# Performance work log

Hardware: AMD Instinct MI355X
Metric: run time of the kernel (lower is better)

Reference implementation:

```python
import jax, jax.numpy as jnp
import numpy as np

ALPHA, BETA = 0.5, 0.25
DELTA_AGG, DELTA_DIS = 0.5, 3.0
OHEM_RATIO = 3
MAX_INST = 8  # instance ids in [0, MAX_INST); 0 = background
NEG_INF = -1e10


def _safe_norm(sq):
    # sqrt with zero-safe gradient; returns 0 where sq == 0
    return jnp.sqrt(jnp.where(sq > 0, sq, 1.0)) * (sq > 0)


def _agg_dis_single(sim, gt_text, gt_kernel):
    # sim: [4, N] float, gt_text/gt_kernel: [N] int32 instance ids
    lab = jnp.arange(1, MAX_INST)                                  # [K]
    kmask = (gt_kernel[None, :] == lab[:, None]).astype(sim.dtype)  # [K, N]
    tmask = gt_text[None, :] == lab[:, None]                        # [K, N] bool
    kcount = kmask.sum(1)
    tcount = tmask.sum(1).astype(sim.dtype)
    valid = (kcount > 0) & (tcount > 0)                             # [K]
    # per-instance kernel centroid G_kernel: masked segment mean of sim vectors
    G = (kmask @ sim.T) / jnp.maximum(kcount, 1.0)[:, None]         # [K, 4]
    # loss_agg: distance of each text pixel's sim vector to its kernel centroid
    diff = sim.T[None, :, :] - G[:, None, :]                        # [K, N, 4]
    d = _safe_norm(jnp.sum(diff * diff, -1))                        # [K, N]
    D = jnp.square(jnp.maximum(d - DELTA_AGG, 0.0))
    per_inst = jnp.sum(jnp.log1p(D) * tmask, 1) / jnp.maximum(tcount, 1.0)
    n_valid = jnp.sum(valid)
    loss_agg = jnp.sum(jnp.where(valid, per_inst, 0.0)) / jnp.maximum(n_valid, 1).astype(sim.dtype)
    # loss_dis: pairwise discrimination between valid kernel centroids
    gd = G[:, None, :] - G[None, :, :]                              # [K, K, 4]
    gnorm = _safe_norm(jnp.sum(gd * gd, -1))
    Dij = jnp.square(jnp.maximum(DELTA_DIS - gnorm, 0.0))
    K = MAX_INST - 1
    idx = jnp.arange(K)
    pair = valid[:, None] & valid[None, :] & (idx[:, None] < idx[None, :])
    s = jnp.sum(jnp.where(pair, jnp.log1p(Dij), 0.0))
    denom = (n_valid * (n_valid - 1)).astype(sim.dtype)  # matches torch: n*(n-1), not #pairs
    loss_dis = jnp.where(n_valid > 1, s / jnp.maximum(denom, 1.0), 0.0)
    return loss_agg, loss_dis


def _ohem_single(score, gt, tm):
    # score/tm: [N] float, gt: [N] int — all flattened
    pos = gt > 0.5
    pos_num = jnp.sum(pos) - jnp.sum(pos & (tm <= 0.5))
    neg = ~pos
    neg_total = jnp.sum(neg)
    neg_num = jnp.minimum(pos_num * OHEM_RATIO, neg_total)
    neg_scores = jnp.where(neg, score, NEG_INF)
    sorted_desc = -jnp.sort(-neg_scores)
    threshold = sorted_desc[jnp.maximum(neg_num - 1, 0)]
    sel = (((score >= threshold) | pos) & (tm > 0.5)).astype(tm.dtype)
    fallback = (pos_num == 0) | (neg_num == 0)
    return jnp.where(fallback, tm, sel)


def _dice(inp, tgt, mask):
    # inp: [B, N] logits, tgt: [B, N] (binarized at 0.5), mask: [B, N]
    p = jax.nn.sigmoid(inp) * mask
    t = (tgt > 0.5).astype(p.dtype) * mask
    a = jnp.sum(p * t, 1)
    b = jnp.sum(p * p, 1) + 1e-3
    c = jnp.sum(t * t, 1) + 1e-3
    return 1.0 - 2.0 * a / (b + c)


def _pan_loss(outputs, labels, training_masks):
    B = outputs.shape[0]
    texts = outputs[:, 0].reshape(B, -1)
    kernels = outputs[:, 1].reshape(B, -1)
    sim = outputs[:, 2:].reshape(B, 4, -1)
    gt_texts = labels[:, 0].reshape(B, -1)
    gt_kernels = labels[:, 1].reshape(B, -1)
    tm = training_masks.reshape(B, -1)

    loss_aggs, loss_diss = jax.vmap(_agg_dis_single)(sim, gt_texts, gt_kernels)

    # OHEM mask is computed on detached scores in the original (numpy round-trip)
    sel_text = jax.vmap(_ohem_single)(jax.lax.stop_gradient(texts), gt_texts, tm)
    loss_texts = _dice(texts, gt_texts, sel_text)

    sel_kernel = jax.lax.stop_gradient(
        ((jax.nn.sigmoid(texts) > 0.5) & (tm > 0.5)).astype(texts.dtype))
    loss_kernels = _dice(kernels, gt_kernels, sel_kernel)

    loss_text = loss_texts.mean()
    loss_kernel = loss_kernels.mean()
    loss_agg = loss_aggs.mean()
    loss_dis = loss_diss.mean()
    loss_all = loss_text + ALPHA * loss_kernel + BETA * (loss_agg + loss_dis)
    return loss_all, loss_text, loss_kernel, loss_agg, loss_dis


def setup_inputs() -> dict:
    key = jax.random.key(0)
    k1, k2, k3 = jax.random.split(key, 3)
    B, H, W = 8, 640, 640
    outputs = jax.random.normal(k1, (B, 6, H, W), dtype=jnp.float32)
    labels = jax.random.randint(k2, (B, 2, H, W), 0, MAX_INST).astype(jnp.int32)
    training_masks = jax.random.uniform(k3, (B, H, W), dtype=jnp.float32)
    return {"outputs": outputs, "labels": labels, "training_masks": training_masks}


def reference(outputs, labels, training_masks):
    return _pan_loss(outputs, labels, training_masks)
```

## Files before the change

kernel.cpp:

```cpp
#include <hip/hip_runtime.h>

#define NPIX 409600
#define NB 8

constexpr int OFF_H0   = 0;
constexpr int OFF_H1   = 2048;
constexpr int OFF_H2   = 4096;
constexpr int OFF_KC   = 5120;
constexpr int OFF_TC   = 5128;
constexpr int OFF_KS   = 5136;
constexpr int OFF_AGG  = 5168;
constexpr int OFF_CPOS = 5176;
constexpr int OFF_CPOSM= 5177;
constexpr int OFF_KN   = 5178;
constexpr int OFF_KNF  = 5179;
constexpr int OFF_FALL = 5180;
constexpr int OFF_NV   = 5181;
constexpr int OFF_VM   = 5182;
constexpr int OFF_LDIS = 5183;
constexpr int OFF_BTN  = 5184;
constexpr int OFF_PFX0 = 5185;
constexpr int OFF_K1   = 5186;
constexpr int OFF_PFX22= 5187;
constexpr int OFF_K2   = 5188;
constexpr int OFF_DICE = 5190;
constexpr int PER_BATCH= 5248;
constexpr int KEYS_BASE= NB * PER_BATCH;
constexpr int HDR_WORDS= NB * PER_BATCH;

__device__ __forceinline__ unsigned mapf(float s) {
  unsigned b = __float_as_uint(s);
  return (b & 0x80000000u) ? ~b : (b | 0x80000000u);
}
__device__ __forceinline__ float unmapf(unsigned u) {
  return __uint_as_float((u & 0x80000000u) ? (u & 0x7FFFFFFFu) : ~u);
}
__device__ __forceinline__ float sigf(float x) {
  return __fdividef(1.f, 1.f + __expf(-x));
}
__device__ __forceinline__ float wredf(float v) {
#pragma unroll
  for (int m = 32; m >= 1; m >>= 1) v += __shfl_xor(v, m, 64);
  return v;
}
__device__ __forceinline__ unsigned wredu(unsigned v) {
#pragma unroll
  for (int m = 32; m >= 1; m >>= 1) v += (unsigned)__shfl_xor((int)v, m, 64);
  return v;
}

__global__ __launch_bounds__(256) void kZ(unsigned* __restrict__ ws) {
  int i = blockIdx.x * 256 + threadIdx.x;
  if (i < HDR_WORDS) ws[i] = 0u;
}

__global__ __launch_bounds__(256) void kXS(const float* __restrict__ out_,
                                           const int* __restrict__ lab_,
                                           const float* __restrict__ tm_,
                                           unsigned* __restrict__ ws) {
  const int b = blockIdx.y;
  unsigned* wsb = ws + (size_t)b * PER_BATCH;
  float* wsbf = (float*)wsb;
  __shared__ __align__(16) unsigned shm[2384];
  const int tid = threadIdx.x, lane = tid & 63, w = tid >> 6;

  if (blockIdx.x < 200) {
    const int bx = blockIdx.x;
    unsigned* sh_h   = shm;
    unsigned* shScan = shm + 2048;
    unsigned* shTC   = shm + 2304;
    float*    shRed  = (float*)(shm + 2332);
    unsigned* shC    = shm + 2368;
    unsigned* shBase = shm + 2376;
    for (int i = tid; i < 2048; i += 256) sh_h[i] = 0u;
    __syncthreads();

    const float4* tx = (const float4*)(out_ + (size_t)b * 6 * NPIX);
    const float4* kr = (const float4*)(out_ + (size_t)b * 6 * NPIX + (size_t)NPIX);
    const int4* gt = (const int4*)(lab_ + (size_t)b * 2 * NPIX);
    const int4* gk = (const int4*)(lab_ + (size_t)b * 2 * NPIX + NPIX);
    const float4* tmv = (const float4*)(tm_ + (size_t)b * NPIX);

    unsigned cpos = 0, cposm = 0, vmask = 0, fmask = 0;
    unsigned tcq[7];
#pragma unroll
    for (int k = 0; k < 7; ++k) tcq[k] = 0u;
    unsigned kreg[8];
    float at = 0.f, btp = 0.f, ct = 0.f, atf = 0.f, btf = 0.f, ctf = 0.f;
    float ak = 0.f, bk = 0.f, ck = 0.f;

#pragma unroll
    for (int it = 0; it < 2; ++it) {
      const int i = it * 51200 + bx * 256 + tid;
      float4 t4 = tx[i]; float4 q4 = kr[i]; int4 g4 = gt[i]; int4 k4 = gk[i]; float4 m4 = tmv[i];
#pragma unroll
      for (int j = 0; j < 4; ++j) {
        float tv = ((const float*)&t4)[j];
        float kv = ((const float*)&q4)[j];
        int gtv = ((const int*)&g4)[j];
        int gkv = ((const int*)&k4)[j];
        float mv = ((const float*)&m4)[j];
        bool pos = gtv > 0;
        bool mh = mv > 0.5f;
        cpos += pos;
        cposm += (pos && !mh);
        unsigned key = mapf(tv);
        kreg[it * 4 + j] = key;
        float sig = sigf(tv);
        if (!pos) {
          vmask |= 1u << (it * 4 + j);
          if (mh) fmask |= 1u << (it * 4 + j);
          atomicAdd(&sh_h[key >> 21], 1u);
        } else if (mh) {
          at += sig; btp += sig * sig; ct += 1.f;
        }
#pragma unroll
        for (int k = 0; k < 7; ++k)
          tcq[k] += (gtv == k + 1);
        float sm = sig * mv;
        btf += sm * sm;
        if (pos) { atf += sm * mv; ctf += mv * mv; }
        if ((tv > 0.f) && mh) {
          float sk = sigf(kv);
          bk += sk * sk;
          if (gkv > 0) { ak += sk; ck += 1.f; }
        }
      }
    }

    unsigned r = wredu(cpos), r2 = wredu(cposm);
    if (lane == 0) { shC[w * 2] = r; shC[w * 2 + 1] = r2; }
#pragma unroll
    for (int k = 0; k < 7; ++k) {
      unsigned rt = wredu(tcq[k]);
      if (lane == 0) shTC[w * 7 + k] = rt;
    }
    float v9[9] = {at, btp, ct, atf, btf, ctf, ak, bk, ck};
#pragma unroll
    for (int q = 0; q < 9; ++q) {
      float f = wredf(v9[q]);
      if (lane == 0) shRed[w * 9 + q] = f;
    }

    unsigned cnt = (unsigned)__popc(vmask), cntF = (unsigned)__popc(fmask);
    shScan[tid] = cnt | (cntF << 16);
    __syncthreads();
#pragma unroll
    for (int off = 1; off < 256; off <<= 1) {
      unsigned vv = (tid >= off) ? shScan[tid - off] : 0u;
      __syncthreads();
      shScan[tid] += vv;
      __syncthreads();
    }
    if (tid == 0) {
      unsigned tot = shScan[255];
      shBase[0] = atomicAdd(&wsb[OFF_KN], tot & 0xFFFFu);
      shBase[1] = atomicAdd(&wsb[OFF_KNF], tot >> 16);
    }
    for (int i = tid; i < 2048; i += 256) {
      unsigned h = sh_h[i]; if (h) atomicAdd(&wsb[OFF_H0 + i], h);
    }
    if (tid < 7) {
      unsigned s = shTC[tid] + shTC[7 + tid] + shTC[14 + tid] + shTC[21 + tid];
      if (s) atomicAdd(&wsb[OFF_TC + 1 + tid], s);
    } else if (tid >= 16 && tid < 25) {
      int q = tid - 16;
      float s = shRed[q] + shRed[9 + q] + shRed[18 + q] + shRed[27 + q];
      atomicAdd(&wsbf[OFF_DICE + q], s);
    } else if (tid == 30) {
      atomicAdd(&wsb[OFF_CPOS], shC[0] + shC[2] + shC[4] + shC[6]);
    } else if (tid == 31) {
      atomicAdd(&wsb[OFF_CPOSM], shC[1] + shC[3] + shC[5] + shC[7]);
    }
    __syncthreads();
    unsigned gA = shBase[0] + (shScan[tid] & 0xFFFFu) - cnt;
    unsigned gF = shBase[1] + (shScan[tid] >> 16) - cntF;
    unsigned* keys = ws + KEYS_BASE + (size_t)b * NPIX;
#pragma unroll
    for (int s = 0; s < 8; ++s)
      if (vmask & (1u << s)) { keys[gA] = kreg[s]; ++gA; }
#pragma unroll
    for (int s = 0; s < 8; ++s)
      if (fmask & (1u << s)) { keys[NPIX - 1 - gF] = kreg[s]; ++gF; }
  } else {
    const bool lo = blockIdx.x < 328;
    const int bx = lo ? (blockIdx.x - 200) : (blockIdx.x - 328);
    float* shSred = (float*)shm;
    unsigned* shScnt = shm + 64;

    const float4* sa = (const float4*)(out_ + (size_t)b * 6 * NPIX + (size_t)(lo ? 2 : 4) * NPIX);
    const float4* sb = (const float4*)(out_ + (size_t)b * 6 * NPIX + (size_t)(lo ? 3 : 5) * NPIX);
    const int4* gkk = (const int4*)(lab_ + (size_t)b * 2 * NPIX + NPIX);

    float ka[7], kb2[7];
    unsigned kcq[7];
#pragma unroll
    for (int k = 0; k < 7; ++k) { ka[k] = 0.f; kb2[k] = 0.f; kcq[k] = 0u; }

    const int nv = NPIX / 4;
    for (int i = bx * 256 + tid; i < nv; i += 128 * 256) {
      int4 k4 = gkk[i];
      float4 a0 = sa[i], a1 = sb[i];
#pragma unroll
      for (int j = 0; j < 4; ++j) {
        int gkv = ((const int*)&k4)[j];
        float va = ((const float*)&a0)[j];
        float vb = ((const float*)&a1)[j];
#pragma unroll
        for (int k = 0; k < 7; ++k) {
          bool m = (gkv == k + 1);
          float sel = m ? 1.f : 0.f;
          ka[k] += sel * va;
          kb2[k] += sel * vb;
          kcq[k] += m;
        }
      }
    }

#pragma unroll
    for (int k = 0; k < 7; ++k) {
      float fa = wredf(ka[k]);
      float fb = wredf(kb2[k]);
      if (lane == 0) { shSred[w * 14 + k] = fa; shSred[w * 14 + 7 + k] = fb; }
      if (lo) {
        unsigned rc = wredu(kcq[k]);
        if (lane == 0) shScnt[w * 7 + k] = rc;
      }
    }
    __syncthreads();
    if (tid < 14) {
      int k = tid % 7, c = tid / 7;
      float s = shSred[c * 7 + k] + shSred[14 + c * 7 + k] +
                shSred[28 + c * 7 + k] + shSred[42 + c * 7 + k];
      if (s != 0.f)
        atomicAdd(&wsbf[OFF_KS + (k + 1) * 4 + (lo ? 0 : 2) + c], s);
    } else if (lo && tid >= 16 && tid < 23) {
      int k = tid - 16;
      unsigned s = shScnt[k] + shScnt[7 + k] + shScnt[14 + k] + shScnt[21 + k];
      if (s) atomicAdd(&wsb[OFF_KC + 1 + k], s);
    }
  }
}

__global__ __launch_bounds__(256) void kGB(const float* __restrict__ out_,
                                           const int* __restrict__ lab_,
                                           unsigned* __restrict__ ws) {
  const int b = blockIdx.y;
  unsigned* wsb = ws + (size_t)b * PER_BATCH;
  float* wsbf = (float*)wsb;
  const int tid = threadIdx.x, lane = tid & 63, w = tid >> 6;

  if (blockIdx.x < 200) {
    __shared__ float sG[32];
    __shared__ float sAgg[4 * 7];
    const int bx = blockIdx.x;
    if (tid < 32) {
      int inst = tid >> 2, c = tid & 3;
      float g = 0.f;
      if (inst >= 1) {
        unsigned kc = wsb[OFF_KC + inst];
        g = wsbf[OFF_KS + inst * 4 + c] / fmaxf((float)kc, 1.f);
      }
      sG[tid] = g;
    }
    __syncthreads();
    const int4* gt = (const int4*)(lab_ + (size_t)b * 2 * NPIX);
    const float4* s0 = (const float4*)(out_ + (size_t)b * 6 * NPIX + 2 * (size_t)NPIX);
    const float4* s1 = (const float4*)(out_ + (size_t)b * 6 * NPIX + 3 * (size_t)NPIX);
    const float4* s2 = (const float4*)(out_ + (size_t)b * 6 * NPIX + 4 * (size_t)NPIX);
    const float4* s3 = (const float4*)(out_ + (size_t)b * 6 * NPIX + 5 * (size_t)NPIX);
    float agg[7];
#pragma unroll
    for (int k = 0; k < 7; ++k) agg[k] = 0.f;
#pragma unroll
    for (int it = 0; it < 2; ++it) {
      const int i = it * 51200 + bx * 256 + tid;
      int4 g4 = gt[i];
      float4 a0 = s0[i], a1 = s1[i], a2 = s2[i], a3 = s3[i];
#pragma unroll
      for (int j = 0; j < 4; ++j) {
        int gtv = ((const int*)&g4)[j];
        bool pos = gtv > 0;
        int kk = pos ? gtv : 0;
        float d0 = ((const float*)&a0)[j] - sG[kk * 4 + 0];
        float d1 = ((const float*)&a1)[j] - sG[kk * 4 + 1];
        float d2 = ((const float*)&a2)[j] - sG[kk * 4 + 2];
        float d3 = ((const float*)&a3)[j] - sG[kk * 4 + 3];
        float sq = d0 * d0 + d1 * d1 + d2 * d2 + d3 * d3;
        float d = (sq > 0.f) ? sqrtf(sq) : 0.f;
        float dd = fmaxf(d - 0.5f, 0.f);
        float lg = pos ? __logf(1.f + dd * dd) : 0.f;
#pragma unroll
        for (int k = 0; k < 7; ++k) agg[k] += (gtv == k + 1) ? lg : 0.f;
      }
    }
#pragma unroll
    for (int k = 0; k < 7; ++k) {
      float f = wredf(agg[k]);
      if (lane == 0) sAgg[w * 7 + k] = f;
    }
    __syncthreads();
    if (tid < 7) {
      float s = sAgg[tid] + sAgg[7 + tid] + sAgg[14 + tid] + sAgg[21 + tid];
      if (s != 0.f) atomicAdd(&wsbf[OFF_AGG + 1 + tid], s);
    }
  } else {
    const int bb = blockIdx.x - 200;
    __shared__ unsigned S[256];
    __shared__ unsigned sh_h1[2048];
    __shared__ unsigned sh_k, sh_pfx0;
    __shared__ int sh_fall;
    if (tid == 0) {
      unsigned cpos = wsb[OFF_CPOS], cposm = wsb[OFF_CPOSM];
      long posnum = (long)cpos - (long)cposm;
      long cneg = (long)NPIX - (long)cpos;
      long negnum = posnum * 3; if (negnum > cneg) negnum = cneg;
      int fall = (posnum == 0) || (negnum == 0);
      wsb[OFF_FALL] = (unsigned)fall;
      sh_fall = fall; sh_k = (unsigned)negnum;
      float G[8][4];
      unsigned nvv = 0, vm = 0;
      for (int k = 1; k < 8; ++k) {
        unsigned kc = wsb[OFF_KC + k], tc = wsb[OFF_TC + k];
        float inv = 1.f / fmaxf((float)kc, 1.f);
        for (int c = 0; c < 4; ++c) G[k][c] = wsbf[OFF_KS + k * 4 + c] * inv;
        if (kc > 0 && tc > 0) { vm |= 1u << k; ++nvv; }
      }
      wsb[OFF_NV] = nvv; wsb[OFF_VM] = vm;
      float s = 0.f;
      for (int i = 1; i < 8; ++i) {
        if (!((vm >> i) & 1)) continue;
        for (int j = i + 1; j < 8; ++j) {
          if (!((vm >> j) & 1)) continue;
          float sq = 0.f;
          for (int c = 0; c < 4; ++c) { float d = G[i][c] - G[j][c]; sq += d * d; }
          float gn = (sq > 0.f) ? sqrtf(sq) : 0.f;
          float dd = fmaxf(3.0f - gn, 0.f);
          s += log1pf(dd * dd);
        }
      }
      float denom = (float)(nvv * (nvv > 0 ? nvv - 1u : 0u));
      wsbf[OFF_LDIS] = (nvv > 1) ? (s / fmaxf(denom, 1.f)) : 0.f;
    }
    __syncthreads();
    if (sh_fall) return;
    unsigned myp = 0;
#pragma unroll
    for (int j = 0; j < 8; ++j) myp += wsb[OFF_H0 + tid * 8 + j];
    S[tid] = myp;
    __syncthreads();
#pragma unroll
    for (int off = 1; off < 256; off <<= 1) {
      unsigned v = (tid + off < 256) ? S[tid + off] : 0u;
      __syncthreads();
      S[tid] += v;
      __syncthreads();
    }
    {
      unsigned k = sh_k;
      unsigned suf = S[tid], sufn = suf - myp;
      if (suf >= k && sufn < k) {
        unsigned kk = k - sufn;
        unsigned cum2 = 0; int bin = tid * 8;
#pragma unroll
        for (int j = 7; j >= 0; --j) {
          unsigned h = wsb[OFF_H0 + tid * 8 + j]; cum2 += h;
          if (cum2 >= kk) { bin = tid * 8 + j; kk -= (cum2 - h); break; }
        }
        sh_pfx0 = (unsigned)bin;
        wsb[OFF_PFX0] = (unsigned)bin;
        wsb[OFF_K1] = kk;
      }
    }
    __syncthreads();
    const unsigned pfx = sh_pfx0;
    const unsigned kn = wsb[OFF_KN];
    for (int i = tid; i < 2048; i += 256) sh_h1[i] = 0u;
    __syncthreads();
    const unsigned* keys = ws + KEYS_BASE + (size_t)b * NPIX;
    for (unsigned i = bb * 256u + tid; i < kn; i += 16u * 256u) {
      unsigned key = keys[i];
      if ((key >> 21) == pfx) atomicAdd(&sh_h1[(key >> 10) & 0x7FFu], 1u);
    }
    __syncthreads();
    for (int i = tid; i < 2048; i += 256) {
      unsigned v = sh_h1[i]; if (v) atomicAdd(&wsb[OFF_H1 + i], v);
    }
  }
}

__global__ __launch_bounds__(256) void kCD(unsigned* __restrict__ ws) {
  const int b = blockIdx.y;
  unsigned* wsb = ws + (size_t)b * PER_BATCH;
  if (wsb[OFF_FALL]) return;
  __shared__ unsigned S[256];
  __shared__ unsigned sh_h2[1024];
  __shared__ unsigned sh_p22;
  const int tid = threadIdx.x;
  unsigned myp = 0;
#pragma unroll
  for (int j = 0; j < 8; ++j) myp += wsb[OFF_H1 + tid * 8 + j];
  S[tid] = myp;
  __syncthreads();
#pragma unroll
  for (int off = 1; off < 256; off <<= 1) {
    unsigned v = (tid + off < 256) ? S[tid + off] : 0u;
    __syncthreads();
    S[tid] += v;
    __syncthreads();
  }
  {
    unsigned k = wsb[OFF_K1];
    unsigned suf = S[tid], sufn = suf - myp;
    if (suf >= k && sufn < k) {
      unsigned kk = k - sufn;
      unsigned cum2 = 0; int bin = tid * 8;
#pragma unroll
      for (int j = 7; j >= 0; --j) {
        unsigned h = wsb[OFF_H1 + tid * 8 + j]; cum2 += h;
        if (cum2 >= kk) { bin = tid * 8 + j; kk -= (cum2 - h); break; }
      }
      unsigned p22 = (wsb[OFF_PFX0] << 11) | (unsigned)bin;
      sh_p22 = p22;
      wsb[OFF_PFX22] = p22;
      wsb[OFF_K2] = kk;
    }
  }
  __syncthreads();
  const unsigned pfx22 = sh_p22;
  const unsigned kn = wsb[OFF_KN];
  for (int i = tid; i < 1024; i += 256) sh_h2[i] = 0u;
  __syncthreads();
  const unsigned* keys = ws + KEYS_BASE + (size_t)b * NPIX;
  for (unsigned i = blockIdx.x * 256u + tid; i < kn; i += 16u * 256u) {
    unsigned key = keys[i];
    if ((key >> 10) == pfx22) atomicAdd(&sh_h2[key & 0x3FFu], 1u);
  }
  __syncthreads();
  for (int i = tid; i < 1024; i += 256) {
    unsigned v = sh_h2[i]; if (v) atomicAdd(&wsb[OFF_H2 + i], v);
  }
}

__global__ __launch_bounds__(256) void kEF(unsigned* __restrict__ ws) {
  const int b = blockIdx.y;
  unsigned* wsb = ws + (size_t)b * PER_BATCH;
  float* wsbf = (float*)wsb;
  if (wsb[OFF_FALL]) return;
  __shared__ unsigned S[256];
  __shared__ unsigned sh_thk;
  __shared__ float sF[4];
  const int tid = threadIdx.x, lane = tid & 63, w = tid >> 6;
  unsigned myp = 0;
#pragma unroll
  for (int j = 0; j < 4; ++j) myp += wsb[OFF_H2 + tid * 4 + j];
  S[tid] = myp;
  __syncthreads();
#pragma unroll
  for (int off = 1; off < 256; off <<= 1) {
    unsigned v = (tid + off < 256) ? S[tid + off] : 0u;
    __syncthreads();
    S[tid] += v;
    __syncthreads();
  }
  {
    unsigned k = wsb[OFF_K2];
    unsigned suf = S[tid], sufn = suf - myp;
    if (suf >= k && sufn < k) {
      unsigned kk = k - sufn;
      unsigned cum2 = 0; int bin = tid * 4;
#pragma unroll
      for (int j = 3; j >= 0; --j) {
        unsigned h = wsb[OFF_H2 + tid * 4 + j]; cum2 += h;
        if (cum2 >= kk) { bin = tid * 4 + j; break; }
      }
      sh_thk = (wsb[OFF_PFX22] << 10) | (unsigned)bin;
    }
  }
  __syncthreads();
  const unsigned thkey = sh_thk;
  const unsigned knF = wsb[OFF_KNF];
  const unsigned* listB = ws + KEYS_BASE + (size_t)b * NPIX + (NPIX - knF);
  float part = 0.f;
  for (unsigned i = blockIdx.x * 256u + tid; i < knF; i += 16u * 256u) {
    unsigned key = listB[i];
    if (key >= thkey) {
      float sg = sigf(unmapf(key));
      part += sg * sg;
    }
  }
  part = wredf(part);
  if (lane == 0) sF[w] = part;
  __syncthreads();
  if (tid == 0) {
    float s = sF[0] + sF[1] + sF[2] + sF[3];
    if (s != 0.f) atomicAdd(&wsbf[OFF_BTN], s);
  }
}

__global__ void kH(const unsigned* __restrict__ ws, float* __restrict__ out) {
  __shared__ float sv[4][8];
  const int b = threadIdx.x;
  if (b < 8) {
    const unsigned* wsb = ws + (size_t)b * PER_BATCH;
    const float* wsbf = (const float*)wsb;
    int fall = (int)wsb[OFF_FALL];
    float at, bt, ct;
    if (fall) {
      at = wsbf[OFF_DICE + 3]; bt = wsbf[OFF_DICE + 4]; ct = wsbf[OFF_DICE + 5];
    } else {
      at = wsbf[OFF_DICE + 0];
      bt = wsbf[OFF_DICE + 1] + wsbf[OFF_BTN];
      ct = wsbf[OFF_DICE + 2];
    }
    float lt = 1.f - 2.f * at / ((bt + 1e-3f) + (ct + 1e-3f));
    float ak = wsbf[OFF_DICE + 6], bk = wsbf[OFF_DICE + 7] + 1e-3f, ck = wsbf[OFF_DICE + 8] + 1e-3f;
    float lk = 1.f - 2.f * ak / (bk + ck);
    unsigned vm = wsb[OFF_VM], nvv = wsb[OFF_NV];
    float s = 0.f;
    for (int k = 1; k < 8; ++k)
      if ((vm >> k) & 1) s += wsbf[OFF_AGG + k] / fmaxf((float)wsb[OFF_TC + k], 1.f);
    float la = s / fmaxf((float)nvv, 1.f);
    float ld = wsbf[OFF_LDIS];
    sv[0][b] = lt; sv[1][b] = lk; sv[2][b] = la; sv[3][b] = ld;
  }
  __syncthreads();
  if (threadIdx.x == 0) {
    float mt = 0.f, mk = 0.f, ma = 0.f, md = 0.f;
    for (int i = 0; i < 8; ++i) { mt += sv[0][i]; mk += sv[1][i]; ma += sv[2][i]; md += sv[3][i]; }
    mt *= 0.125f; mk *= 0.125f; ma *= 0.125f; md *= 0.125f;
    out[0] = mt + 0.5f * mk + 0.25f * (ma + md);
    out[1] = mt;
    out[2] = mk;
    out[3] = ma;
    out[4] = md;
  }
}

extern "C" void kernel_launch(void* const* d_in, const int* in_sizes, int n_in,
                              void* d_out, int out_size, void* d_ws, size_t ws_size,
                              hipStream_t stream) {
  const float* outputs = (const float*)d_in[0];
  const int* labels = (const int*)d_in[1];
  const float* tm = (const float*)d_in[2];
  unsigned* ws = (unsigned*)d_ws;
  float* out = (float*)d_out;

  dim3 blk(256);
  kZ<<<(HDR_WORDS + 255) / 256, blk, 0, stream>>>(ws);
  kXS<<<dim3(456, NB), blk, 0, stream>>>(outputs, labels, tm, ws);
  kGB<<<dim3(216, NB), blk, 0, stream>>>(outputs, labels, ws);
  kCD<<<dim3(16, NB), blk, 0, stream>>>(ws);
  kEF<<<dim3(16, NB), blk, 0, stream>>>(ws);
  kH<<<1, 64, 0, stream>>>(ws, out);
}
```

Baseline: 91.37 us.

## Halve stats blocks, pack instance counts into nibble accumulators, hoist loads

```diff
diff --git a/kernel.cpp b/kernel.cpp
--- a/kernel.cpp
+++ b/kernel.cpp
@@ -64,7 +64,7 @@
   __shared__ __align__(16) unsigned shm[2384];
   const int tid = threadIdx.x, lane = tid & 63, w = tid >> 6;
 
-  if (blockIdx.x < 200) {
+  if (blockIdx.x < 100) {
     const int bx = blockIdx.x;
     unsigned* sh_h   = shm;
     unsigned* shScan = shm + 2048;
@@ -81,58 +81,67 @@
     const int4* gk = (const int4*)(lab_ + (size_t)b * 2 * NPIX + NPIX);
     const float4* tmv = (const float4*)(tm_ + (size_t)b * NPIX);
 
-    unsigned cpos = 0, cposm = 0, vmask = 0, fmask = 0;
-    unsigned tcq[7];
-#pragma unroll
-    for (int k = 0; k < 7; ++k) tcq[k] = 0u;
-    unsigned kreg[8];
+    unsigned cposm = 0, vmask = 0, fmask = 0;
+    unsigned long long tnib = 0ull;
+    unsigned kreg[16];
     float at = 0.f, btp = 0.f, ct = 0.f, atf = 0.f, btf = 0.f, ctf = 0.f;
     float ak = 0.f, bk = 0.f, ck = 0.f;
 
 #pragma unroll
-    for (int it = 0; it < 2; ++it) {
-      const int i = it * 51200 + bx * 256 + tid;
-      float4 t4 = tx[i]; float4 q4 = kr[i]; int4 g4 = gt[i]; int4 k4 = gk[i]; float4 m4 = tmv[i];
-#pragma unroll
-      for (int j = 0; j < 4; ++j) {
-        float tv = ((const float*)&t4)[j];
-        float kv = ((const float*)&q4)[j];
-        int gtv = ((const int*)&g4)[j];
-        int gkv = ((const int*)&k4)[j];
-        float mv = ((const float*)&m4)[j];
-        bool pos = gtv > 0;
-        bool mh = mv > 0.5f;
-        cpos += pos;
-        cposm += (pos && !mh);
-        unsigned key = mapf(tv);
-        kreg[it * 4 + j] = key;
-        float sig = sigf(tv);
-        if (!pos) {
-          vmask |= 1u << (it * 4 + j);
-          if (mh) fmask |= 1u << (it * 4 + j);
-          atomicAdd(&sh_h[key >> 21], 1u);
-        } else if (mh) {
-          at += sig; btp += sig * sig; ct += 1.f;
+    for (int g = 0; g < 2; ++g) {
+      const int i0 = (2 * g) * 25600 + bx * 256 + tid;
+      const int i1 = (2 * g + 1) * 25600 + bx * 256 + tid;
+      float4 t4a = tx[i0], q4a = kr[i0], m4a = tmv[i0];
+      int4 g4a = gt[i0], k4a = gk[i0];
+      float4 t4b = tx[i1], q4b = kr[i1], m4b = tmv[i1];
+      int4 g4b = gt[i1], k4b = gk[i1];
+#pragma unroll
+      for (int h = 0; h < 2; ++h) {
+        const float4& t4 = h ? t4b : t4a;
+        const float4& q4 = h ? q4b : q4a;
+        const float4& m4 = h ? m4b : m4a;
+        const int4& g4 = h ? g4b : g4a;
+        const int4& k4 = h ? k4b : k4a;
+#pragma unroll
+        for (int j = 0; j < 4; ++j) {
+          float tv = ((const float*)&t4)[j];
+          float kv = ((const float*)&q4)[j];
+          int gtv = ((const int*)&g4)[j];
+          int gkv = ((const int*)&k4)[j];
+          float mv = ((const float*)&m4)[j];
+          bool pos = gtv > 0;
+          bool mh = mv > 0.5f;
+          cposm += (pos && !mh);
+          tnib += 1ull << ((unsigned)(gtv & 7) << 3);
+          unsigned key = mapf(tv);
+          int slot = g * 8 + h * 4 + j;
+          kreg[slot] = key;
+          float sig = sigf(tv);
+          if (!pos) {
+            vmask |= 1u << slot;
+            if (mh) fmask |= 1u << slot;
+            atomicAdd(&sh_h[key >> 21], 1u);
+          } else if (mh) {
+            at += sig; btp += sig * sig; ct += 1.f;
+          }
+          float sm = sig * mv;
+          btf += sm * sm;
+          if (pos) { atf += sm * mv; ctf += mv * mv; }
+          if ((tv > 0.f) && mh) {
+            float sk = sigf(kv);
+            bk += sk * sk;
+            if (gkv > 0) { ak += sk; ck += 1.f; }
+          }
         }
-#pragma unroll
-        for (int k = 0; k < 7; ++k)
-          tcq[k] += (gtv == k + 1);
-        float sm = sig * mv;
-        btf += sm * sm;
-        if (pos) { atf += sm * mv; ctf += mv * mv; }
-        if ((tv > 0.f) && mh) {
-          float sk = sigf(kv);
-          bk += sk * sk;
-          if (gkv > 0) { ak += sk; ck += 1.f; }
-        }
-      }
-    }
-
+      }
+    }
+
+    unsigned cpos = 16u - (unsigned)(tnib & 0xFFull);
     unsigned r = wredu(cpos), r2 = wredu(cposm);
     if (lane == 0) { shC[w * 2] = r; shC[w * 2 + 1] = r2; }
 #pragma unroll
     for (int k = 0; k < 7; ++k) {
-      unsigned rt = wredu(tcq[k]);
+      unsigned rt = wredu((unsigned)((tnib >> ((k + 1) * 8)) & 0xFFull));
       if (lane == 0) shTC[w * 7 + k] = rt;
     }
     float v9[9] = {at, btp, ct, atf, btf, ctf, ak, bk, ck};
@@ -177,14 +186,14 @@
     unsigned gF = shBase[1] + (shScan[tid] >> 16) - cntF;
     unsigned* keys = ws + KEYS_BASE + (size_t)b * NPIX;
 #pragma unroll
-    for (int s = 0; s < 8; ++s)
+    for (int s = 0; s < 16; ++s)
       if (vmask & (1u << s)) { keys[gA] = kreg[s]; ++gA; }
 #pragma unroll
-    for (int s = 0; s < 8; ++s)
+    for (int s = 0; s < 16; ++s)
       if (fmask & (1u << s)) { keys[NPIX - 1 - gF] = kreg[s]; ++gF; }
   } else {
-    const bool lo = blockIdx.x < 328;
-    const int bx = lo ? (blockIdx.x - 200) : (blockIdx.x - 328);
+    const bool lo = blockIdx.x < 228;
+    const int bx = lo ? (blockIdx.x - 100) : (blockIdx.x - 228);
     float* shSred = (float*)shm;
     unsigned* shScnt = shm + 64;
 
@@ -193,26 +202,45 @@
     const int4* gkk = (const int4*)(lab_ + (size_t)b * 2 * NPIX + NPIX);
 
     float ka[7], kb2[7];
-    unsigned kcq[7];
-#pragma unroll
-    for (int k = 0; k < 7; ++k) { ka[k] = 0.f; kb2[k] = 0.f; kcq[k] = 0u; }
+    unsigned long long knib = 0ull;
+#pragma unroll
+    for (int k = 0; k < 7; ++k) { ka[k] = 0.f; kb2[k] = 0.f; }
 
     const int nv = NPIX / 4;
-    for (int i = bx * 256 + tid; i < nv; i += 128 * 256) {
-      int4 k4 = gkk[i];
-      float4 a0 = sa[i], a1 = sb[i];
+    const int stride = 128 * 256;
+    for (int i0 = bx * 256 + tid; i0 < nv; i0 += 2 * stride) {
+      const int i1 = i0 + stride;
+      const bool has1 = i1 < nv;
+      int4 k4a = gkk[i0];
+      float4 a0a = sa[i0], a1a = sb[i0];
+      int4 k4b; float4 a0b, a1b;
+      if (has1) { k4b = gkk[i1]; a0b = sa[i1]; a1b = sb[i1]; }
 #pragma unroll
       for (int j = 0; j < 4; ++j) {
-        int gkv = ((const int*)&k4)[j];
-        float va = ((const float*)&a0)[j];
-        float vb = ((const float*)&a1)[j];
+        int gkv = ((const int*)&k4a)[j];
+        float va = ((const float*)&a0a)[j];
+        float vb = ((const float*)&a1a)[j];
+        knib += 1ull << ((unsigned)(gkv & 7) << 3);
 #pragma unroll
         for (int k = 0; k < 7; ++k) {
-          bool m = (gkv == k + 1);
-          float sel = m ? 1.f : 0.f;
+          float sel = (gkv == k + 1) ? 1.f : 0.f;
           ka[k] += sel * va;
           kb2[k] += sel * vb;
-          kcq[k] += m;
+        }
+      }
+      if (has1) {
+#pragma unroll
+        for (int j = 0; j < 4; ++j) {
+          int gkv = ((const int*)&k4b)[j];
+          float va = ((const float*)&a0b)[j];
+          float vb = ((const float*)&a1b)[j];
+          knib += 1ull << ((unsigned)(gkv & 7) << 3);
+#pragma unroll
+          for (int k = 0; k < 7; ++k) {
+            float sel = (gkv == k + 1) ? 1.f : 0.f;
+            ka[k] += sel * va;
+            kb2[k] += sel * vb;
+          }
         }
       }
     }
@@ -223,7 +251,7 @@
       float fb = wredf(kb2[k]);
       if (lane == 0) { shSred[w * 14 + k] = fa; shSred[w * 14 + 7 + k] = fb; }
       if (lo) {
-        unsigned rc = wredu(kcq[k]);
+        unsigned rc = wredu((unsigned)((knib >> ((k + 1) * 8)) & 0xFFull));
         if (lane == 0) shScnt[w * 7 + k] = rc;
       }
     }
@@ -272,11 +300,19 @@
     float agg[7];
 #pragma unroll
     for (int k = 0; k < 7; ++k) agg[k] = 0.f;
-#pragma unroll
-    for (int it = 0; it < 2; ++it) {
-      const int i = it * 51200 + bx * 256 + tid;
-      int4 g4 = gt[i];
-      float4 a0 = s0[i], a1 = s1[i], a2 = s2[i], a3 = s3[i];
+    const int i0 = bx * 256 + tid;
+    const int i1 = 51200 + bx * 256 + tid;
+    int4 g4a = gt[i0];
+    float4 a0a = s0[i0], a1a = s1[i0], a2a = s2[i0], a3a = s3[i0];
+    int4 g4b = gt[i1];
+    float4 a0b = s0[i1], a1b = s1[i1], a2b = s2[i1], a3b = s3[i1];
+#pragma unroll
+    for (int h = 0; h < 2; ++h) {
+      const int4& g4 = h ? g4b : g4a;
+      const float4& a0 = h ? a0b : a0a;
+      const float4& a1 = h ? a1b : a1a;
+      const float4& a2 = h ? a2b : a2a;
+      const float4& a3 = h ? a3b : a3a;
 #pragma unroll
       for (int j = 0; j < 4; ++j) {
         int gtv = ((const int*)&g4)[j];
@@ -548,7 +584,7 @@
 
   dim3 blk(256);
   kZ<<<(HDR_WORDS + 255) / 256, blk, 0, stream>>>(ws);
-  kXS<<<dim3(456, NB), blk, 0, stream>>>(outputs, labels, tm, ws);
+  kXS<<<dim3(356, NB), blk, 0, stream>>>(outputs, labels, tm, ws);
   kGB<<<dim3(216, NB), blk, 0, stream>>>(outputs, labels, ws);
   kCD<<<dim3(16, NB), blk, 0, stream>>>(ws);
   kEF<<<dim3(16, NB), blk, 0, stream>>>(ws);
```

Measured after the change: 82.52 us. 9.7% less time.
